# Performance work log

Measured on AMD Instinct MI355X. Metric: run time of the kernel, lower is better.

Reference implementation:

```python
import jax, jax.numpy as jnp
import numpy as np

T = 10.0            # neuralef_loss_cfg['t']
ALPHA = 0.05        # neuralef_loss_cfg['alpha']
PW_W = 0.1          # pixelwise_adj_weight
PW_DIV = 1.0        # pixelwise_adj_div_factor
K_LIST = ((20, 2.0), (10, 0.1))  # hard-coded in source


def _pdist(x):
    # x: (b, n, d) -> (b, n, n) euclidean distance (torch.cdist)
    sq = jnp.sum(x * x, -1)
    d2 = sq[:, :, None] + sq[:, None, :] - 2.0 * jnp.einsum('bnd,bmd->bnm', x, x)
    return jnp.sqrt(jnp.maximum(d2, 0.0))


def _mutual_knn(feats, k):
    # mutual k-NN boolean adjacency: scatter topk then AND with transpose
    bs, n, _ = feats.shape
    neg = -_pdist(feats)
    neg = jnp.where(jnp.eye(n, dtype=bool), -jnp.inf, neg)
    idx = jax.lax.top_k(neg, k)[1]                       # (bs, n, k)
    res = jnp.zeros((bs, n, n), dtype=bool).at[
        jnp.arange(bs)[:, None, None], jnp.arange(n)[None, :, None], idx].set(True)
    return jnp.logical_and(res, res.transpose(0, 2, 1))


def setup_inputs() -> dict:
    key = jax.random.key(0)
    k1, k2, k3 = jax.random.split(key, 3)
    N, C, K = 8192, 384, 512
    bs, h, w = 8, 32, 32
    FF = jax.random.normal(k1, (N, C), dtype=jnp.float32)
    Psi = jax.random.normal(k2, (N, K), dtype=jnp.float32)
    im = jax.random.uniform(k3, (bs, 3, h, w), dtype=jnp.float32, minval=-1.0, maxval=1.0)
    return {"FF": FF, "Psi": Psi, "im": im}


def reference(FF, Psi, im):
    N = FF.shape[0]
    Psi = Psi * (T / N)
    # --- adjacency (torch.no_grad block) ---
    FFn = FF / jnp.linalg.norm(FF, axis=1, keepdims=True)
    A = FFn @ FFn.T
    A = jnp.where(jnp.eye(N, dtype=bool), 0.0, A)       # fill_diagonal_(0)
    A = jnp.maximum(A, 0.0)                              # thresholded kernel
    # --- pixelwise mutual-kNN adjacency per image ---
    bs, _, h, w = im.shape
    hw = h * w
    im01 = (im + 1.0) * 0.5
    x_ = jnp.tile(jnp.linspace(0.0, 1.0, w), h)          # (hw,)
    y_ = jnp.repeat(jnp.linspace(0.0, 1.0, h), w)        # (hw,)
    feat = im01.reshape(bs, 3, hw).transpose(0, 2, 1) / PW_DIV  # (bs, hw, 3)
    A_p = None
    for k, dw in K_LIST:
        f2 = jnp.concatenate([
            feat,
            jnp.broadcast_to((x_ * dw)[None, :, None], (bs, hw, 1)),
            jnp.broadcast_to((y_ * dw)[None, :, None], (bs, hw, 1)),
        ], -1)
        m = _mutual_knn(f2, k)
        A_p = m if A_p is None else jnp.logical_or(A_p, m)
    # add PW_W * A_p to block-diagonal blocks of A
    A4 = A.reshape(bs, hw, bs, hw)
    bi = jnp.arange(bs)
    A4 = A4.at[bi, :, bi, :].add(PW_W * A_p.astype(A.dtype))
    A = A4.reshape(N, N)
    # degree normalization
    D = jax.lax.rsqrt(A.sum(-1) / (N - 1))
    gram = A * D[None, :] * D[:, None]
    # --- neuralef loss ---
    R = Psi.T @ gram @ Psi                               # (K, K)
    R_hat = jax.lax.stop_gradient(Psi).T @ gram @ Psi    # no_sg=False
    loss = -jnp.trace(R)
    reg = jnp.sum(jnp.triu(R_hat ** 2, 1)) * ALPHA
    return jnp.stack([loss, reg])
```

## Files before the change

kernel.cpp:

```cpp
#include <hip/hip_runtime.h>
#include <hip/hip_bf16.h>

#define NN 8192
#define CC 384
#define KD 512
#define HWP 1024

typedef __attribute__((ext_vector_type(8))) short bf16x8;
typedef __attribute__((ext_vector_type(4))) float f32x4;

static constexpr float T_OVER_N = 10.0f / 8192.0f;

__device__ __forceinline__ float bf2f(unsigned short u) {
    union { unsigned int i; float f; } x;
    x.i = ((unsigned int)u) << 16;
    return x.f;
}
__device__ __forceinline__ unsigned short f2bf(float f) {
    __hip_bfloat16 h = __float2bfloat16(f);
    unsigned short u;
    __builtin_memcpy(&u, &h, sizeof(u));
    return u;
}

__device__ __forceinline__ void wait_vm8() {
    asm volatile("s_waitcnt vmcnt(8)" ::: "memory");
    __builtin_amdgcn_sched_barrier(0);
}
__device__ __forceinline__ void wait_vm0() {
    asm volatile("s_waitcnt vmcnt(0)" ::: "memory");
    __builtin_amdgcn_sched_barrier(0);
}
__device__ __forceinline__ void rawbar() {
    __builtin_amdgcn_s_barrier();
    __builtin_amdgcn_sched_barrier(0);
}

__device__ __forceinline__ void stage_tile(const unsigned short* __restrict__ src, long ld,
                                           int k0, unsigned short* lds) {
    const int t = threadIdx.x;
    #pragma unroll
    for (int i = 0; i < 4; ++i) {
        int slot = i * 256 + t;
        int row = slot >> 3;
        int cl = (slot & 7) ^ (row & 7);
        const unsigned short* g = src + (long)row * ld + k0 + cl * 8;
        __builtin_amdgcn_global_load_lds((const __attribute__((address_space(1))) void*)g,
                                         (__attribute__((address_space(3))) void*)(lds + (size_t)slot * 8),
                                         16, 0, 0);
    }
}

__device__ __forceinline__ bf16x8 read_frag(const unsigned short* lds, int r, int chunk) {
    int byte = (r << 7) + (((chunk ^ r) & 7) << 4) + ((chunk & ~7) << 4);
    return *(const bf16x8*)((const char*)lds + byte);
}

__device__ __forceinline__ void gemm_step(const unsigned short* As, const unsigned short* Bs,
                                          int arl, int brl, int lhi, f32x4 (&acc)[4][4]) {
    #pragma unroll
    for (int ks = 0; ks < 2; ++ks) {
        bf16x8 a[4], b[4];
        #pragma unroll
        for (int m = 0; m < 4; ++m) a[m] = read_frag(As, arl + m * 16, ks * 4 + lhi);
        #pragma unroll
        for (int n = 0; n < 4; ++n) b[n] = read_frag(Bs, brl + n * 16, ks * 4 + lhi);
        #pragma unroll
        for (int m = 0; m < 4; ++m)
            #pragma unroll
            for (int n = 0; n < 4; ++n)
                acc[m][n] = __builtin_amdgcn_mfma_f32_16x16x32_bf16(a[m], b[n], acc[m][n], 0, 0, 0);
    }
}

__global__ __launch_bounds__(128) void k_normalize(const float* __restrict__ FF,
                                                   unsigned short* __restrict__ FFnb) {
    int row = blockIdx.x;
    int tid = threadIdx.x;
    const float* src = FF + (size_t)row * CC;
    float v0 = src[tid], v1 = src[tid + 128], v2 = src[tid + 256];
    float s = v0 * v0 + v1 * v1 + v2 * v2;
    #pragma unroll
    for (int off = 32; off > 0; off >>= 1) s += __shfl_down(s, off, 64);
    __shared__ float ls[2];
    if ((tid & 63) == 0) ls[tid >> 6] = s;
    __syncthreads();
    float inv = 1.0f / sqrtf(ls[0] + ls[1]);
    unsigned short* dst = FFnb + (size_t)row * CC;
    dst[tid] = f2bf(v0 * inv);
    dst[tid + 128] = f2bf(v1 * inv);
    dst[tid + 256] = f2bf(v2 * inv);
}

__global__ __launch_bounds__(256) void k_knn(const float* __restrict__ im,
                                             unsigned char* __restrict__ res20,
                                             unsigned char* __restrict__ res10) {
    const int lane = threadIdx.x & 63;
    const int id = blockIdx.x * 4 + (threadIdx.x >> 6);
    const int v = id & 1;
    const int rest = id >> 1;
    const int p = rest & 1023;
    const int b = rest >> 10;
    const float dw = v ? 0.1f : 2.0f;
    const int kneigh = v ? 10 : 20;
    const float* im0 = im + (size_t)b * 3 * HWP;
    const float scale = dw * (1.0f / 31.0f);
    float rf0 = (im0[p] + 1.f) * 0.5f;
    float rf1 = (im0[HWP + p] + 1.f) * 0.5f;
    float rf2 = (im0[2 * HWP + p] + 1.f) * 0.5f;
    float rx = (float)(p & 31) * scale;
    float ry = (float)(p >> 5) * scale;
    unsigned long long key[16];
    #pragma unroll
    for (int e = 0; e < 16; ++e) {
        int q = e * 64 + lane;
        float f0 = (im0[q] + 1.f) * 0.5f - rf0;
        float f1 = (im0[HWP + q] + 1.f) * 0.5f - rf1;
        float f2 = (im0[2 * HWP + q] + 1.f) * 0.5f - rf2;
        float fx = (float)(q & 31) * scale - rx;
        float fy = (float)(q >> 5) * scale - ry;
        float d = f0 * f0 + f1 * f1 + f2 * f2 + fx * fx + fy * fy;
        unsigned int db = __float_as_uint(d);
        key[e] = (q == p) ? ~0ull : ((((unsigned long long)db) << 10) | (unsigned int)q);
    }
    unsigned int selmask = 0;
    for (int it = 0; it < kneigh; ++it) {
        unsigned long long m = key[0];
        #pragma unroll
        for (int e = 1; e < 16; ++e) m = (key[e] < m) ? key[e] : m;
        #pragma unroll
        for (int off = 1; off < 64; off <<= 1) {
            unsigned long long o = __shfl_xor((unsigned long long)m, off, 64);
            m = (o < m) ? o : m;
        }
        int q = (int)(m & 1023u);
        if ((q & 63) == lane) {
            int e = q >> 6;
            selmask |= 1u << e;
            key[e] = ~0ull;
        }
    }
    unsigned char* dst = (v ? res10 : res20) + ((size_t)(b * HWP + p)) * HWP;
    #pragma unroll
    for (int e = 0; e < 16; ++e) dst[e * 64 + lane] = (unsigned char)((selmask >> e) & 1u);
}

__global__ __launch_bounds__(256, 2) void k_gram_off(const unsigned short* __restrict__ FFnb,
                                                     unsigned short* __restrict__ A,
                                                     float* __restrict__ rowsum) {
    __shared__ __align__(16) unsigned short Sh[4][8192];
    int s = ((blockIdx.x & 7) * 260) + (blockIdx.x >> 3);
    int ti = 0, rem = s;
    while (rem >= 64 - ti) { rem -= 64 - ti; ++ti; }
    const int tj = ti + rem;
    if ((ti >> 3) == (tj >> 3)) return;
    const int row0 = ti * 128, col0 = tj * 128;
    const int tid = threadIdx.x, l = tid & 63, wid = tid >> 6;
    const int wr = (wid >> 1) * 64, wc = (wid & 1) * 64;
    const int arl = wr + (l & 15), brl = wc + (l & 15), lhi = l >> 4;
    f32x4 z = {0.f, 0.f, 0.f, 0.f};
    f32x4 acc[4][4];
    #pragma unroll
    for (int m = 0; m < 4; ++m)
        #pragma unroll
        for (int n = 0; n < 4; ++n) acc[m][n] = z;

    stage_tile(FFnb + (long)row0 * CC, CC, 0, Sh[0]);
    stage_tile(FFnb + (long)col0 * CC, CC, 0, Sh[1]);
    for (int t = 0; t < 6; ++t) {
        const int cur = t & 1, nxt = cur ^ 1;
        if (t + 1 < 6) {
            stage_tile(FFnb + (long)row0 * CC, CC, (t + 1) * 64, Sh[2 * nxt]);
            stage_tile(FFnb + (long)col0 * CC, CC, (t + 1) * 64, Sh[2 * nxt + 1]);
            wait_vm8();
        } else {
            wait_vm0();
        }
        rawbar();
        gemm_step(Sh[2 * cur], Sh[2 * cur + 1], arl, brl, lhi, acc);
        rawbar();
    }
    float rs[4][4];
    float cs[4] = {0.f, 0.f, 0.f, 0.f};
    #pragma unroll
    for (int m = 0; m < 4; ++m)
        #pragma unroll
        for (int r = 0; r < 4; ++r) rs[m][r] = 0.f;
    char* Mir = (char*)Sh;
    #pragma unroll
    for (int m = 0; m < 4; ++m) {
        #pragma unroll
        for (int n = 0; n < 4; ++n) {
            #pragma unroll
            for (int r = 0; r < 4; ++r) {
                int il = wr + m * 16 + lhi * 4 + r;
                int jl = wc + n * 16 + (l & 15);
                float vv = fmaxf(acc[m][n][r], 0.f);
                unsigned short u = f2bf(vv);
                A[(long)(row0 + il) * NN + col0 + jl] = u;
                rs[m][r] += vv;
                cs[n] += vv;
                *(unsigned short*)(Mir + jl * 256 + ((il * 2) ^ ((jl & 15) << 4))) = u;
            }
        }
    }
    #pragma unroll
    for (int m = 0; m < 4; ++m)
        #pragma unroll
        for (int r = 0; r < 4; ++r) {
            float p = rs[m][r];
            #pragma unroll
            for (int off = 1; off < 16; off <<= 1) p += __shfl_xor(p, off, 64);
            if ((l & 15) == 0) atomicAdd(&rowsum[row0 + wr + m * 16 + lhi * 4 + r], p);
        }
    #pragma unroll
    for (int n = 0; n < 4; ++n) {
        float p = cs[n];
        p += __shfl_xor(p, 16, 64);
        p += __shfl_xor(p, 32, 64);
        if (l < 16) atomicAdd(&rowsum[col0 + wc + n * 16 + l], p);
    }
    __syncthreads();
    #pragma unroll
    for (int p8 = 0; p8 < 8; ++p8) {
        int idx = p8 * 256 + tid;
        int jl = idx >> 4;
        int cl = idx & 15;
        int sl = cl ^ (jl & 15);
        bf16x8 v = *(const bf16x8*)(Mir + jl * 256 + sl * 16);
        *(bf16x8*)(A + (long)(col0 + jl) * NN + row0 + cl * 8) = v;
    }
}

__global__ __launch_bounds__(256, 2) void k_gram_diag(const unsigned short* __restrict__ FFnb,
                                                      const unsigned char* __restrict__ res20,
                                                      const unsigned char* __restrict__ res10,
                                                      unsigned short* __restrict__ A,
                                                      float* __restrict__ rowsum) {
    __shared__ __align__(16) unsigned short Sh[4][8192];
    int s = ((blockIdx.x & 7) * 36) + (blockIdx.x >> 3);
    int band = s / 36, p = s % 36;
    int a = 0, rem = p;
    while (rem >= 8 - a) { rem -= 8 - a; ++a; }
    const int ti = band * 8 + a, tj = band * 8 + a + rem;
    const int row0 = ti * 128, col0 = tj * 128;
    const int tid = threadIdx.x, l = tid & 63, wid = tid >> 6;
    const int wr = (wid >> 1) * 64, wc = (wid & 1) * 64;
    const int arl = wr + (l & 15), brl = wc + (l & 15), lhi = l >> 4;
    f32x4 z = {0.f, 0.f, 0.f, 0.f};
    f32x4 acc[4][4];
    #pragma unroll
    for (int m = 0; m < 4; ++m)
        #pragma unroll
        for (int n = 0; n < 4; ++n) acc[m][n] = z;

    stage_tile(FFnb + (long)row0 * CC, CC, 0, Sh[0]);
    stage_tile(FFnb + (long)col0 * CC, CC, 0, Sh[1]);
    for (int t = 0; t < 6; ++t) {
        const int cur = t & 1, nxt = cur ^ 1;
        if (t + 1 < 6) {
            stage_tile(FFnb + (long)row0 * CC, CC, (t + 1) * 64, Sh[2 * nxt]);
            stage_tile(FFnb + (long)col0 * CC, CC, (t + 1) * 64, Sh[2 * nxt + 1]);
            wait_vm8();
        } else {
            wait_vm0();
        }
        rawbar();
        gemm_step(Sh[2 * cur], Sh[2 * cur + 1], arl, brl, lhi, acc);
        rawbar();
    }
    const bool offd = (ti != tj);
    const long mbase = ((long)band) << 20;
    float rs[4][4];
    float cs[4] = {0.f, 0.f, 0.f, 0.f};
    #pragma unroll
    for (int m = 0; m < 4; ++m)
        #pragma unroll
        for (int r = 0; r < 4; ++r) rs[m][r] = 0.f;
    char* Mir = (char*)Sh;
    #pragma unroll
    for (int m = 0; m < 4; ++m) {
        #pragma unroll
        for (int n = 0; n < 4; ++n) {
            #pragma unroll
            for (int r = 0; r < 4; ++r) {
                int il = wr + m * 16 + lhi * 4 + r;
                int jl = wc + n * 16 + (l & 15);
                int gi = row0 + il, gj = col0 + jl;
                float vv = acc[m][n][r];
                vv = (gi == gj) ? 0.f : fmaxf(vv, 0.f);
                int li = gi & 1023, lj = gj & 1023;
                unsigned char mm = (unsigned char)(
                    (res20[mbase + (long)li * HWP + lj] & res20[mbase + (long)lj * HWP + li]) |
                    (res10[mbase + (long)li * HWP + lj] & res10[mbase + (long)lj * HWP + li]));
                vv += 0.1f * (float)mm;
                unsigned short u = f2bf(vv);
                A[(long)gi * NN + gj] = u;
                rs[m][r] += vv;
                if (offd) {
                    cs[n] += vv;
                    *(unsigned short*)(Mir + jl * 256 + ((il * 2) ^ ((jl & 15) << 4))) = u;
                }
            }
        }
    }
    #pragma unroll
    for (int m = 0; m < 4; ++m)
        #pragma unroll
        for (int r = 0; r < 4; ++r) {
            float p2 = rs[m][r];
            #pragma unroll
            for (int off = 1; off < 16; off <<= 1) p2 += __shfl_xor(p2, off, 64);
            if ((l & 15) == 0) atomicAdd(&rowsum[row0 + wr + m * 16 + lhi * 4 + r], p2);
        }
    if (offd) {
        #pragma unroll
        for (int n = 0; n < 4; ++n) {
            float p2 = cs[n];
            p2 += __shfl_xor(p2, 16, 64);
            p2 += __shfl_xor(p2, 32, 64);
            if (l < 16) atomicAdd(&rowsum[col0 + wc + n * 16 + l], p2);
        }
        __syncthreads();
        #pragma unroll
        for (int p8 = 0; p8 < 8; ++p8) {
            int idx = p8 * 256 + tid;
            int jl = idx >> 4;
            int cl = idx & 15;
            int sl = cl ^ (jl & 15);
            bf16x8 v = *(const bf16x8*)(Mir + jl * 256 + sl * 16);
            *(bf16x8*)(A + (long)(col0 + jl) * NN + row0 + cl * 8) = v;
        }
    }
}

__global__ __launch_bounds__(256) void k_d(const float* __restrict__ rowsum,
                                           float* __restrict__ Dv) {
    int i = blockIdx.x * 256 + threadIdx.x;
    Dv[i] = 1.0f / sqrtf(rowsum[i] * (1.0f / 8191.0f));
}

__global__ __launch_bounds__(256) void k_psiT(const float* __restrict__ Psi,
                                              const float* __restrict__ Dv,
                                              unsigned short* __restrict__ PaT,
                                              unsigned short* __restrict__ PsT) {
    __shared__ unsigned short tile[128][72];
    __shared__ float Dvs[64];
    const int j0 = blockIdx.x * 64;
    const int n0 = blockIdx.y * 128;
    const int t = threadIdx.x;
    if (t < 64) Dvs[t] = Dv[j0 + t];
    #pragma unroll
    for (int i = 0; i < 8; ++i) {
        int jl = i * 8 + (t >> 5);
        int c4 = (t & 31) * 4;
        float4 vv = *(const float4*)(Psi + (size_t)(j0 + jl) * KD + n0 + c4);
        tile[c4 + 0][jl] = f2bf(vv.x * T_OVER_N);
        tile[c4 + 1][jl] = f2bf(vv.y * T_OVER_N);
        tile[c4 + 2][jl] = f2bf(vv.z * T_OVER_N);
        tile[c4 + 3][jl] = f2bf(vv.w * T_OVER_N);
    }
    __syncthreads();
    const int nl = t >> 1;
    const int jh = (t & 1) * 32;
    unsigned short pa[32], ps[32];
    #pragma unroll
    for (int jj = 0; jj < 32; ++jj) {
        unsigned short u = tile[nl][jh + jj];
        pa[jj] = u;
        ps[jj] = f2bf(bf2f(u) * Dvs[jh + jj]);
    }
    unsigned short* dpa = PaT + (size_t)(n0 + nl) * NN + j0 + jh;
    unsigned short* dps = PsT + (size_t)(n0 + nl) * NN + j0 + jh;
    #pragma unroll
    for (int c = 0; c < 4; ++c) {
        *(bf16x8*)(dpa + c * 8) = *(const bf16x8*)(pa + c * 8);
        *(bf16x8*)(dps + c * 8) = *(const bf16x8*)(ps + c * 8);
    }
}

__global__ __launch_bounds__(256, 2) void k_yt2(const unsigned short* __restrict__ A,
                                                const unsigned short* __restrict__ PsT,
                                                const float* __restrict__ Dv,
                                                unsigned short* __restrict__ W) {
    __shared__ __align__(16) unsigned short Sh[4][8192];
    int slot = (blockIdx.x & 7) * 32 + (blockIdx.x >> 3);
    const int it = slot >> 2, nt = slot & 3;
    const int row0 = it * 128, col0 = nt * 128;
    const int tid = threadIdx.x, l = tid & 63, wid = tid >> 6;
    const int wr = (wid >> 1) * 64, wc = (wid & 1) * 64;
    const int arl = wr + (l & 15), brl = wc + (l & 15), lhi = l >> 4;
    f32x4 z = {0.f, 0.f, 0.f, 0.f};
    f32x4 acc[4][4];
    #pragma unroll
    for (int m = 0; m < 4; ++m)
        #pragma unroll
        for (int n = 0; n < 4; ++n) acc[m][n] = z;

    stage_tile(A + (long)row0 * NN, NN, 0, Sh[0]);
    stage_tile(PsT + (long)col0 * NN, NN, 0, Sh[1]);
    for (int t = 0; t < 128; ++t) {
        const int cur = t & 1, nxt = cur ^ 1;
        if (t + 1 < 128) {
            int k1 = (t + 1) * 64;
            stage_tile(A + (long)row0 * NN, NN, k1, Sh[2 * nxt]);
            stage_tile(PsT + (long)col0 * NN, NN, k1, Sh[2 * nxt + 1]);
            wait_vm8();
        } else {
            wait_vm0();
        }
        rawbar();
        gemm_step(Sh[2 * cur], Sh[2 * cur + 1], arl, brl, lhi, acc);
        rawbar();
    }
    #pragma unroll
    for (int m = 0; m < 4; ++m) {
        #pragma unroll
        for (int r = 0; r < 4; ++r) {
            int gi = row0 + wr + m * 16 + lhi * 4 + r;
            float dvi = Dv[gi];
            #pragma unroll
            for (int n = 0; n < 4; ++n) {
                int gj = col0 + wc + n * 16 + (l & 15);
                W[(long)gi * KD + gj] = f2bf(acc[m][n][r] * dvi);
            }
        }
    }
}

__global__ __launch_bounds__(256) void k_wt(const unsigned short* __restrict__ W,
                                            unsigned short* __restrict__ YT) {
    __shared__ unsigned short t64[64][80];
    const int i0 = blockIdx.x * 64;
    const int n0 = blockIdx.y * 64;
    const int t = threadIdx.x;
    int il = t >> 2, nc = (t & 3) * 16;
    bf16x8 v0 = *(const bf16x8*)(W + (long)(i0 + il) * KD + n0 + nc);
    bf16x8 v1 = *(const bf16x8*)(W + (long)(i0 + il) * KD + n0 + nc + 8);
    #pragma unroll
    for (int e = 0; e < 8; ++e) {
        t64[nc + e][il] = (unsigned short)v0[e];
        t64[nc + 8 + e][il] = (unsigned short)v1[e];
    }
    __syncthreads();
    int nl = t >> 2, jc = (t & 3) * 16;
    bf16x8 o0 = *(const bf16x8*)(&t64[nl][jc]);
    bf16x8 o1 = *(const bf16x8*)(&t64[nl][jc + 8]);
    *(bf16x8*)(YT + (long)(n0 + nl) * NN + i0 + jc) = o0;
    *(bf16x8*)(YT + (long)(n0 + nl) * NN + i0 + jc + 8) = o1;
}

__global__ __launch_bounds__(256, 2) void k_r(const unsigned short* __restrict__ PaT,
                                              const unsigned short* __restrict__ YT,
                                              float* __restrict__ R) {
    static const int t1tab[10] = {0,0,0,0,1,1,1,2,2,3};
    static const int t2tab[10] = {0,1,2,3,1,2,3,2,3,3};
    const int t1 = t1tab[blockIdx.x], t2 = t2tab[blockIdx.x], kz = blockIdx.y;
    __shared__ __align__(16) unsigned short Sh[4][8192];
    const int row0 = t1 * 128, col0 = t2 * 128;
    const int tid = threadIdx.x, l = tid & 63, wid = tid >> 6;
    const int wr = (wid >> 1) * 64, wc = (wid & 1) * 64;
    const int arl = wr + (l & 15), brl = wc + (l & 15), lhi = l >> 4;
    f32x4 z = {0.f, 0.f, 0.f, 0.f};
    f32x4 acc[4][4];
    #pragma unroll
    for (int m = 0; m < 4; ++m)
        #pragma unroll
        for (int n = 0; n < 4; ++n) acc[m][n] = z;

    const int kbeg = kz * 1024;
    stage_tile(PaT + (long)row0 * NN, NN, kbeg, Sh[0]);
    stage_tile(YT + (long)col0 * NN, NN, kbeg, Sh[1]);
    for (int t = 0; t < 16; ++t) {
        const int cur = t & 1, nxt = cur ^ 1;
        if (t + 1 < 16) {
            int k1 = kbeg + (t + 1) * 64;
            stage_tile(PaT + (long)row0 * NN, NN, k1, Sh[2 * nxt]);
            stage_tile(YT + (long)col0 * NN, NN, k1, Sh[2 * nxt + 1]);
            wait_vm8();
        } else {
            wait_vm0();
        }
        rawbar();
        gemm_step(Sh[2 * cur], Sh[2 * cur + 1], arl, brl, lhi, acc);
        rawbar();
    }
    #pragma unroll
    for (int m = 0; m < 4; ++m) {
        #pragma unroll
        for (int n = 0; n < 4; ++n) {
            #pragma unroll
            for (int r = 0; r < 4; ++r) {
                int gk1 = row0 + wr + m * 16 + lhi * 4 + r;
                int gk2 = col0 + wc + n * 16 + (l & 15);
                atomicAdd(&R[(long)gk1 * KD + gk2], acc[m][n][r]);
            }
        }
    }
}

__global__ __launch_bounds__(256) void k_tri(const float* __restrict__ R,
                                             float* __restrict__ acc2) {
    float tr = 0.f, rg = 0.f;
    for (int idx = blockIdx.x * 256 + threadIdx.x; idx < KD * KD; idx += 64 * 256) {
        int k1 = idx >> 9, k2 = idx & 511;
        float v = R[idx];
        if (k1 == k2) tr += v;
        else if (k1 < k2) rg += v * v;
    }
    #pragma unroll
    for (int off = 32; off > 0; off >>= 1) {
        tr += __shfl_down(tr, off, 64);
        rg += __shfl_down(rg, off, 64);
    }
    __shared__ float lt[4], lr[4];
    int tid = threadIdx.x;
    if ((tid & 63) == 0) { lt[tid >> 6] = tr; lr[tid >> 6] = rg; }
    __syncthreads();
    if (tid == 0) {
        atomicAdd(&acc2[0], lt[0] + lt[1] + lt[2] + lt[3]);
        atomicAdd(&acc2[1], lr[0] + lr[1] + lr[2] + lr[3]);
    }
}

__global__ void k_fin(const float* __restrict__ acc2, float* __restrict__ out) {
    out[0] = -acc2[0];
    out[1] = 0.05f * acc2[1];
}

extern "C" void kernel_launch(void* const* d_in, const int* in_sizes, int n_in,
                              void* d_out, int out_size, void* d_ws, size_t ws_size,
                              hipStream_t stream) {
    const float* FF  = (const float*)d_in[0];
    const float* Psi = (const float*)d_in[1];
    const float* im  = (const float*)d_in[2];
    float* out = (float*)d_out;
    char* ws = (char*)d_ws;
    size_t off = 0;
    auto alloc = [&](size_t bytes) {
        size_t o = off;
        off += (bytes + 255) & ~(size_t)255;
        return o;
    };
    unsigned short* FFnb  = (unsigned short*)(ws + alloc((size_t)NN * CC * 2));
    unsigned char* res20  = (unsigned char*)(ws + alloc((size_t)8 * HWP * HWP));
    unsigned char* res10  = (unsigned char*)(ws + alloc((size_t)8 * HWP * HWP));
    float* rowsum         = (float*)(ws + alloc((size_t)NN * 4));
    float* Dv             = (float*)(ws + alloc((size_t)NN * 4));
    unsigned short* PaT   = (unsigned short*)(ws + alloc((size_t)KD * NN * 2));
    unsigned short* PsT   = (unsigned short*)(ws + alloc((size_t)KD * NN * 2));
    unsigned short* W     = (unsigned short*)(ws + alloc((size_t)NN * KD * 2));
    unsigned short* YT    = (unsigned short*)(ws + alloc((size_t)KD * NN * 2));
    float* R              = (float*)(ws + alloc((size_t)KD * KD * 4));
    float* acc2           = (float*)(ws + alloc(256));
    unsigned short* A     = (unsigned short*)(ws + alloc((size_t)NN * NN * 2));

    hipMemsetAsync(rowsum, 0, (size_t)NN * 4, stream);
    hipMemsetAsync(R, 0, (size_t)KD * KD * 4, stream);
    hipMemsetAsync(acc2, 0, 8, stream);

    k_normalize<<<NN, 128, 0, stream>>>(FF, FFnb);
    k_knn<<<4096, 256, 0, stream>>>(im, res20, res10);
    k_gram_off<<<2080, 256, 0, stream>>>(FFnb, A, rowsum);
    k_gram_diag<<<288, 256, 0, stream>>>(FFnb, res20, res10, A, rowsum);
    k_d<<<NN / 256, 256, 0, stream>>>(rowsum, Dv);
    k_psiT<<<dim3(128, 4), 256, 0, stream>>>(Psi, Dv, PaT, PsT);
    k_yt2<<<256, 256, 0, stream>>>(A, PsT, Dv, W);
    k_wt<<<dim3(NN / 64, KD / 64), 256, 0, stream>>>(W, YT);
    k_r<<<dim3(10, 8), 256, 0, stream>>>(PaT, YT, R);
    k_tri<<<64, 256, 0, stream>>>(R, acc2);
    k_fin<<<1, 1, 0, stream>>>(acc2, out);
}
```

Baseline: 315.7 us.

## Deepen A*Psi GEMM pipeline to four LDS stages and double R split-K

The main GEMM kernel (A times scaled Psi) moves from a two-buffer LDS pipeline to a four-buffer ring that prefetches three tiles ahead, with matching vmcnt waits, so more global loads are in flight. It now needs 128KB of LDS, so launch bounds drop to one block per CU, giving up occupancy in exchange for deeper prefetch. The R GEMM also doubles its split-K factor (16 chunks of 512) so more blocks run at once, at the cost of more atomic accumulation into R.

```diff
diff --git a/kernel.cpp b/kernel.cpp
--- a/kernel.cpp
+++ b/kernel.cpp
@@ -23,6 +23,14 @@
     return u;
 }
 
+__device__ __forceinline__ void wait_vm24() {
+    asm volatile("s_waitcnt vmcnt(24)" ::: "memory");
+    __builtin_amdgcn_sched_barrier(0);
+}
+__device__ __forceinline__ void wait_vm16() {
+    asm volatile("s_waitcnt vmcnt(16)" ::: "memory");
+    __builtin_amdgcn_sched_barrier(0);
+}
 __device__ __forceinline__ void wait_vm8() {
     asm volatile("s_waitcnt vmcnt(8)" ::: "memory");
     __builtin_amdgcn_sched_barrier(0);
@@ -379,11 +387,12 @@
     }
 }
 
-__global__ __launch_bounds__(256, 2) void k_yt2(const unsigned short* __restrict__ A,
+__global__ __launch_bounds__(256, 1) void k_yt4(const unsigned short* __restrict__ A,
                                                 const unsigned short* __restrict__ PsT,
                                                 const float* __restrict__ Dv,
                                                 unsigned short* __restrict__ W) {
-    __shared__ __align__(16) unsigned short Sh[4][8192];
+    __shared__ __align__(16) unsigned short ShA[4][8192];
+    __shared__ __align__(16) unsigned short ShB[4][8192];
     int slot = (blockIdx.x & 7) * 32 + (blockIdx.x >> 3);
     const int it = slot >> 2, nt = slot & 3;
     const int row0 = it * 128, col0 = nt * 128;
@@ -397,20 +406,29 @@
         #pragma unroll
         for (int n = 0; n < 4; ++n) acc[m][n] = z;
 
-    stage_tile(A + (long)row0 * NN, NN, 0, Sh[0]);
-    stage_tile(PsT + (long)col0 * NN, NN, 0, Sh[1]);
+    const unsigned short* Abase = A + (long)row0 * NN;
+    const unsigned short* Bbase = PsT + (long)col0 * NN;
+    #pragma unroll
+    for (int p = 0; p < 3; ++p) {
+        stage_tile(Abase, NN, p * 64, ShA[p]);
+        stage_tile(Bbase, NN, p * 64, ShB[p]);
+    }
     for (int t = 0; t < 128; ++t) {
-        const int cur = t & 1, nxt = cur ^ 1;
-        if (t + 1 < 128) {
-            int k1 = (t + 1) * 64;
-            stage_tile(A + (long)row0 * NN, NN, k1, Sh[2 * nxt]);
-            stage_tile(PsT + (long)col0 * NN, NN, k1, Sh[2 * nxt + 1]);
+        const int cur = t & 3;
+        if (t + 3 < 128) {
+            int k1 = (t + 3) * 64;
+            stage_tile(Abase, NN, k1, ShA[(t + 3) & 3]);
+            stage_tile(Bbase, NN, k1, ShB[(t + 3) & 3]);
+            wait_vm24();
+        } else if (t == 125) {
+            wait_vm16();
+        } else if (t == 126) {
             wait_vm8();
         } else {
             wait_vm0();
         }
         rawbar();
-        gemm_step(Sh[2 * cur], Sh[2 * cur + 1], arl, brl, lhi, acc);
+        gemm_step(ShA[cur], ShB[cur], arl, brl, lhi, acc);
         rawbar();
     }
     #pragma unroll
@@ -468,12 +486,12 @@
         #pragma unroll
         for (int n = 0; n < 4; ++n) acc[m][n] = z;
 
-    const int kbeg = kz * 1024;
+    const int kbeg = kz * 512;
     stage_tile(PaT + (long)row0 * NN, NN, kbeg, Sh[0]);
     stage_tile(YT + (long)col0 * NN, NN, kbeg, Sh[1]);
-    for (int t = 0; t < 16; ++t) {
+    for (int t = 0; t < 8; ++t) {
         const int cur = t & 1, nxt = cur ^ 1;
-        if (t + 1 < 16) {
+        if (t + 1 < 8) {
             int k1 = kbeg + (t + 1) * 64;
             stage_tile(PaT + (long)row0 * NN, NN, k1, Sh[2 * nxt]);
             stage_tile(YT + (long)col0 * NN, NN, k1, Sh[2 * nxt + 1]);
@@ -565,9 +583,9 @@
     k_gram_diag<<<288, 256, 0, stream>>>(FFnb, res20, res10, A, rowsum);
     k_d<<<NN / 256, 256, 0, stream>>>(rowsum, Dv);
     k_psiT<<<dim3(128, 4), 256, 0, stream>>>(Psi, Dv, PaT, PsT);
-    k_yt2<<<256, 256, 0, stream>>>(A, PsT, Dv, W);
+    k_yt4<<<256, 256, 0, stream>>>(A, PsT, Dv, W);
     k_wt<<<dim3(NN / 64, KD / 64), 256, 0, stream>>>(W, YT);
-    k_r<<<dim3(10, 8), 256, 0, stream>>>(PaT, YT, R);
+    k_r<<<dim3(10, 16), 256, 0, stream>>>(PaT, YT, R);
     k_tri<<<64, 256, 0, stream>>>(R, acc2);
     k_fin<<<1, 1, 0, stream>>>(acc2, out);
 }
```

Result: slower. 367.7 us (+16.4%).
